# Performance work log

Hardware: AMD Instinct MI355X
Metric: run time of the kernel (lower is better)

## Reference

```python
import jax, jax.numpy as jnp
import numpy as np

DIM = 1024
HEADS = 16
DIM_HEAD = 64
B, N = 4, 2048


def setup_inputs() -> dict:
    key = jax.random.key(0)
    ks = jax.random.split(key, 10)
    s = 0.02
    x = jax.random.normal(ks[0], (B, N, DIM), dtype=jnp.float32)
    Wq = jax.random.normal(ks[1], (DIM, DIM), dtype=jnp.float32) * s
    bq = jnp.zeros((DIM,), dtype=jnp.float32)
    Wk = jax.random.normal(ks[2], (DIM, DIM), dtype=jnp.float32) * s
    bk = jnp.zeros((DIM,), dtype=jnp.float32)
    Wv = jax.random.normal(ks[3], (DIM, DIM), dtype=jnp.float32) * s
    bv = jnp.zeros((DIM,), dtype=jnp.float32)
    Wo = jax.random.normal(ks[4], (DIM, DIM), dtype=jnp.float32) * s
    bo = jnp.zeros((DIM,), dtype=jnp.float32)
    # learnable log-temperature, init = log(dim_head ** -0.5)
    log_temp = jnp.array(np.log(DIM_HEAD ** -0.5), dtype=jnp.float32)
    return {"x": x, "Wq": Wq, "bq": bq, "Wk": Wk, "bk": bk,
            "Wv": Wv, "bv": bv, "Wo": Wo, "bo": bo, "log_temp": log_temp}


def reference(x, Wq, bq, Wk, bk, Wv, bv, Wo, bo, log_temp):
    b, n, _ = x.shape
    # projections (dropout is identity at p=0)
    q = x @ Wq + bq
    k = x @ Wk + bk
    v = x @ Wv + bv
    # [b, n, h*d] -> [b, h, n, d]
    def split_heads(t):
        return t.reshape(b, n, HEADS, DIM_HEAD).transpose(0, 2, 1, 3)
    q, k, v = split_heads(q), split_heads(k), split_heads(v)
    # scaled dot-product scores with learnable temperature
    dots = jnp.einsum('bhid,bhjd->bhij', q, k) * jnp.exp(log_temp)
    # mask out self-attention (diagonal) with -finfo.max
    mask_value = -jnp.finfo(dots.dtype).max
    eye = jnp.eye(n, dtype=bool)
    dots = jnp.where(eye, mask_value, dots)
    attn = jax.nn.softmax(dots, axis=-1)
    out = jnp.einsum('bhij,bhjd->bhid', attn, v)
    # [b, h, n, d] -> [b, n, h*d]
    out = out.transpose(0, 2, 1, 3).reshape(b, n, HEADS * DIM_HEAD)
    return out @ Wo + bo
```

## Files before the change

kernel.cpp:

```cpp
#include <hip/hip_runtime.h>
#include <cmath>

typedef __bf16 bf16_t;
typedef __attribute__((ext_vector_type(8))) __bf16 bf16x8;
typedef __attribute__((ext_vector_type(4))) __bf16 bf16x4;
typedef __attribute__((ext_vector_type(4))) float f32x4;

#define SEQ   2048
#define NHEAD 16
#define DHEAD 64
#define NB    4
#define DIMSZ 1024
#define MROWS 8192

__device__ __forceinline__ void async_copy16(const void* g, void* lds) {
  __builtin_amdgcn_global_load_lds(
      (__attribute__((address_space(1))) void*)(g),
      (__attribute__((address_space(3))) void*)(lds), 16, 0, 0);
}

__device__ __forceinline__ f32x4 f32x4_zero() {
  f32x4 v; v[0] = 0.f; v[1] = 0.f; v[2] = 0.f; v[3] = 0.f; return v;
}

__global__ __launch_bounds__(256) void cvt_x(const float* __restrict__ x,
                                             bf16_t* __restrict__ xb) {
  size_t i = ((size_t)blockIdx.x * 256 + threadIdx.x) * 8;
  float4 f0 = *(const float4*)(x + i);
  float4 f1 = *(const float4*)(x + i + 4);
  bf16x8 o;
  o[0] = (__bf16)f0.x; o[1] = (__bf16)f0.y; o[2] = (__bf16)f0.z; o[3] = (__bf16)f0.w;
  o[4] = (__bf16)f1.x; o[5] = (__bf16)f1.y; o[6] = (__bf16)f1.z; o[7] = (__bf16)f1.w;
  *(bf16x8*)(xb + i) = o;
}

__global__ __launch_bounds__(256) void transpose_w(
    const float* __restrict__ W0, const float* __restrict__ W1,
    const float* __restrict__ W2, const float* __restrict__ W3,
    bf16_t* __restrict__ T0, bf16_t* __restrict__ T1,
    bf16_t* __restrict__ T2, bf16_t* __restrict__ T3) {
  const float* W; bf16_t* T;
  switch (blockIdx.z) {
    case 0: W = W0; T = T0; break;
    case 1: W = W1; T = T1; break;
    case 2: W = W2; T = T2; break;
    default: W = W3; T = T3; break;
  }
  __shared__ float t[32][33];
  int tx = threadIdx.x, ty = threadIdx.y;
  int col = blockIdx.x * 32 + tx;
#pragma unroll
  for (int i = 0; i < 4; i++) {
    int row = blockIdx.y * 32 + ty + i * 8;
    t[ty + i * 8][tx] = W[row * DIMSZ + col];
  }
  __syncthreads();
#pragma unroll
  for (int i = 0; i < 4; i++) {
    int n = blockIdx.x * 32 + ty + i * 8;
    int k = blockIdx.y * 32 + tx;
    T[n * DIMSZ + k] = (bf16_t)t[tx][ty + i * 8];
  }
}

__device__ __forceinline__ void gemm_mainloop(
    const bf16_t* __restrict__ A, const bf16_t* __restrict__ Bt,
    int m0, int n0, f32x4 acc[4][4]) {
  __shared__ __attribute__((aligned(16))) bf16_t As[128 * 64];
  __shared__ __attribute__((aligned(16))) bf16_t Bs[128 * 64];
  const int tid = threadIdx.x;
  const int wid = tid >> 6, lane = tid & 63;
  const int quad = lane >> 4, l16 = lane & 15;
  const int wm = wid & 1, wn = wid >> 1;
  const int srow = lane >> 3;
  const int gchunk = (lane & 7) ^ srow;
#pragma unroll
  for (int r = 0; r < 4; r++)
#pragma unroll
    for (int c = 0; c < 4; c++) acc[r][c] = f32x4_zero();

  for (int k0 = 0; k0 < DIMSZ; k0 += 64) {
#pragma unroll
    for (int c2 = 0; c2 < 4; c2++) {
      int row = c2 * 32 + wid * 8 + srow;
      async_copy16(A + (size_t)(m0 + row) * DIMSZ + k0 + gchunk * 8,
                   &As[(c2 * 32 + wid * 8) * 64]);
      async_copy16(Bt + (size_t)(n0 + row) * DIMSZ + k0 + gchunk * 8,
                   &Bs[(c2 * 32 + wid * 8) * 64]);
    }
    __syncthreads();
#pragma unroll
    for (int kk = 0; kk < 2; kk++) {
      bf16x8 af[4], bf[4];
#pragma unroll
      for (int r = 0; r < 4; r++) {
        int row = wm * 64 + r * 16 + l16;
        int slot = (kk * 4 + quad) ^ (row & 7);
        af[r] = *(const bf16x8*)(As + row * 64 + slot * 8);
      }
#pragma unroll
      for (int c = 0; c < 4; c++) {
        int row = wn * 64 + c * 16 + l16;
        int slot = (kk * 4 + quad) ^ (row & 7);
        bf[c] = *(const bf16x8*)(Bs + row * 64 + slot * 8);
      }
#pragma unroll
      for (int r = 0; r < 4; r++)
#pragma unroll
        for (int c = 0; c < 4; c++)
          acc[r][c] = __builtin_amdgcn_mfma_f32_16x16x32_bf16(af[r], bf[c],
                                                              acc[r][c], 0, 0, 0);
    }
    __syncthreads();
  }
}

__global__ __launch_bounds__(256) void gemm_qkv(
    const bf16_t* __restrict__ A,
    const bf16_t* __restrict__ Wt0, const bf16_t* __restrict__ Wt1,
    const bf16_t* __restrict__ Wt2,
    const float* __restrict__ b0, const float* __restrict__ b1,
    const float* __restrict__ b2,
    bf16_t* __restrict__ o0, bf16_t* __restrict__ o1, bf16_t* __restrict__ o2) {
  const bf16_t* Bt; const float* bias; bf16_t* dst;
  if (blockIdx.z == 0)      { Bt = Wt0; bias = b0; dst = o0; }
  else if (blockIdx.z == 1) { Bt = Wt1; bias = b1; dst = o1; }
  else                      { Bt = Wt2; bias = b2; dst = o2; }
  const int m0 = blockIdx.x * 128, n0 = blockIdx.y * 128;
  f32x4 acc[4][4];
  gemm_mainloop(A, Bt, m0, n0, acc);
  const int lane = threadIdx.x & 63, wid = threadIdx.x >> 6;
  const int quad = lane >> 4, l16 = lane & 15;
  const int wm = wid & 1, wn = wid >> 1;
  if (blockIdx.z == 2) {
#pragma unroll
    for (int c = 0; c < 4; c++) {
      int col = n0 + wn * 64 + c * 16 + l16;
      float bv = bias[col];
      int hh = col >> 6, dd = col & 63;
#pragma unroll
      for (int r = 0; r < 4; r++) {
        int row = m0 + wm * 64 + r * 16 + quad * 4;
        int bb = row >> 11, nn = row & (SEQ - 1);
        bf16x4 pk;
#pragma unroll
        for (int rr = 0; rr < 4; rr++) pk[rr] = (__bf16)(acc[r][c][rr] + bv);
        *(bf16x4*)(dst + ((size_t)(bb * NHEAD + hh) * DHEAD + dd) * SEQ + nn) = pk;
      }
    }
  } else {
#pragma unroll
    for (int c = 0; c < 4; c++) {
      int col = n0 + wn * 64 + c * 16 + l16;
      float bv = bias[col];
      int hh = col >> 6, dd = col & 63;
#pragma unroll
      for (int r = 0; r < 4; r++)
#pragma unroll
        for (int rr = 0; rr < 4; rr++) {
          int row = m0 + wm * 64 + r * 16 + quad * 4 + rr;
          int bb = row >> 11, nn = row & (SEQ - 1);
          dst[(((size_t)(bb * NHEAD + hh) * SEQ + nn) << 6) + dd] =
              (bf16_t)(acc[r][c][rr] + bv);
        }
    }
  }
}

__global__ __launch_bounds__(256) void gemm_out(
    const bf16_t* __restrict__ A, const bf16_t* __restrict__ Bt,
    const float* __restrict__ bias, float* __restrict__ dst) {
  const int m0 = blockIdx.x * 128, n0 = blockIdx.y * 128;
  f32x4 acc[4][4];
  gemm_mainloop(A, Bt, m0, n0, acc);
  const int lane = threadIdx.x & 63, wid = threadIdx.x >> 6;
  const int quad = lane >> 4, l16 = lane & 15;
  const int wm = wid & 1, wn = wid >> 1;
#pragma unroll
  for (int c = 0; c < 4; c++) {
    int col = n0 + wn * 64 + c * 16 + l16;
    float bv = bias[col];
#pragma unroll
    for (int r = 0; r < 4; r++)
#pragma unroll
      for (int rr = 0; rr < 4; rr++) {
        int row = m0 + wm * 64 + r * 16 + quad * 4 + rr;
        dst[(size_t)row * DIMSZ + col] = acc[r][c][rr] + bv;
      }
  }
}

__global__ __launch_bounds__(256, 4) void attn_kernel(
    const bf16_t* __restrict__ qh, const bf16_t* __restrict__ kh,
    const bf16_t* __restrict__ vt, bf16_t* __restrict__ ao,
    const float* __restrict__ log_temp) {
  __shared__ __attribute__((aligned(16))) bf16_t Ks[64 * 64];
  __shared__ __attribute__((aligned(16))) bf16_t Vs[64 * 64];
  __shared__ __attribute__((aligned(16))) bf16_t Ps[4][32 * 64];
  const int tid = threadIdx.x;
  const int wid = tid >> 6, lane = tid & 63;
  const int quad = lane >> 4, l16 = lane & 15;
  const int i0 = blockIdx.x * 128;
  const int h = blockIdx.y, b = blockIdx.z;
  const size_t ho = (size_t)(b * NHEAD + h) * SEQ * DHEAD;
  const bf16_t* Q = qh + ho;
  const float ascale = expf(log_temp[0]) * 1.44269504f;
  const float bshift = 16.0f * 1.44269504f;

  const int irow = i0 + wid * 32;
  bf16x8 qf[2][2];
#pragma unroll
  for (int g = 0; g < 2; g++)
#pragma unroll
    for (int jj = 0; jj < 2; jj++)
      qf[g][jj] = *(const bf16x8*)(Q + (size_t)(irow + g * 16 + l16) * DHEAD +
                                   jj * 32 + quad * 8);

  f32x4 oacc[4][2];
#pragma unroll
  for (int c = 0; c < 4; c++)
#pragma unroll
    for (int g = 0; g < 2; g++) oacc[c][g] = f32x4_zero();
  float lsum[2] = {0.f, 0.f};

  const int srow = lane >> 3;
  const int gch = (lane & 7) ^ srow;
  const bf16_t* kg = kh + ho + (size_t)(wid * 8 + srow) * DHEAD + gch * 8;
  const bf16_t* vg = vt + ho + (size_t)(wid * 8 + srow) * SEQ + gch * 8;
  bf16_t* ksd = &Ks[wid * 8 * 64];
  bf16_t* vsd = &Vs[wid * 8 * 64];
  bf16_t* Pw = Ps[wid];
  const int jdiag = i0 + (wid >> 1) * 64;
  const int x7 = l16 & 7;

  for (int j0 = 0; j0 < SEQ; j0 += 64) {
    async_copy16(kg, ksd);
    async_copy16(kg + 32 * DHEAD, ksd + 32 * 64);
    async_copy16(vg, vsd);
    async_copy16(vg + 32 * SEQ, vsd + 32 * 64);
    kg += 64 * DHEAD;
    vg += 64;
    __syncthreads();

    f32x4 st[4][2];
#pragma unroll
    for (int c = 0; c < 4; c++) {
      const int krow = c * 16 + l16;
      bf16x8 kf0 = *(const bf16x8*)(Ks + krow * 64 + ((0 + quad) ^ x7) * 8);
      bf16x8 kf1 = *(const bf16x8*)(Ks + krow * 64 + ((4 + quad) ^ x7) * 8);
#pragma unroll
      for (int g = 0; g < 2; g++) {
        f32x4 s = f32x4_zero();
        s = __builtin_amdgcn_mfma_f32_16x16x32_bf16(kf0, qf[g][0], s, 0, 0, 0);
        s = __builtin_amdgcn_mfma_f32_16x16x32_bf16(kf1, qf[g][1], s, 0, 0, 0);
        st[c][g] = s;
      }
    }

    const bool isdiag = (j0 == jdiag);
#pragma unroll
    for (int g = 0; g < 2; g++) {
      float ls = 0.f;
      const int ig = irow + g * 16 + l16;
#pragma unroll
      for (int c = 0; c < 4; c++) {
        bf16x4 pk;
#pragma unroll
        for (int rr = 0; rr < 4; rr++) {
          float e = __builtin_amdgcn_exp2f(fmaf(st[c][g][rr], ascale, -bshift));
          if (isdiag && (j0 + c * 16 + quad * 4 + rr == ig)) e = 0.f;
          ls += e;
          pk[rr] = (__bf16)e;
        }
        int slot = (2 * c + (quad >> 1)) ^ x7;
        *(bf16x4*)(Pw + (g * 16 + l16) * 64 + slot * 8 + (quad & 1) * 4) = pk;
      }
      lsum[g] += ls;
    }

    bf16x8 pa[2][2];
#pragma unroll
    for (int g = 0; g < 2; g++) {
      pa[g][0] = *(const bf16x8*)(Pw + (g * 16 + l16) * 64 + ((0 + quad) ^ x7) * 8);
      pa[g][1] = *(const bf16x8*)(Pw + (g * 16 + l16) * 64 + ((4 + quad) ^ x7) * 8);
    }
#pragma unroll
    for (int c = 0; c < 4; c++) {
      const int vrow = c * 16 + l16;
      bf16x8 vb0 = *(const bf16x8*)(Vs + vrow * 64 + ((0 + quad) ^ x7) * 8);
      bf16x8 vb1 = *(const bf16x8*)(Vs + vrow * 64 + ((4 + quad) ^ x7) * 8);
#pragma unroll
      for (int g = 0; g < 2; g++) {
        oacc[c][g] = __builtin_amdgcn_mfma_f32_16x16x32_bf16(pa[g][0], vb0,
                                                             oacc[c][g], 0, 0, 0);
        oacc[c][g] = __builtin_amdgcn_mfma_f32_16x16x32_bf16(pa[g][1], vb1,
                                                             oacc[c][g], 0, 0, 0);
      }
    }
    __syncthreads();
  }

#pragma unroll
  for (int g = 0; g < 2; g++) {
    lsum[g] += __shfl_xor(lsum[g], 16);
    lsum[g] += __shfl_xor(lsum[g], 32);
  }
#pragma unroll
  for (int g = 0; g < 2; g++)
#pragma unroll
    for (int rr = 0; rr < 4; rr++) {
      float lr = __shfl(lsum[g], (lane & 48) | (quad * 4 + rr));
      float inv = 1.f / lr;
      int row = irow + g * 16 + quad * 4 + rr;
#pragma unroll
      for (int c = 0; c < 4; c++) {
        ao[(size_t)(b * SEQ + row) * DIMSZ + h * DHEAD + c * 16 + l16] =
            (bf16_t)(oacc[c][g][rr] * inv);
      }
    }
}

extern "C" void kernel_launch(void* const* d_in, const int* in_sizes, int n_in,
                              void* d_out, int out_size, void* d_ws, size_t ws_size,
                              hipStream_t stream) {
  const float* x  = (const float*)d_in[0];
  const float* Wq = (const float*)d_in[1];
  const float* bq = (const float*)d_in[2];
  const float* Wk = (const float*)d_in[3];
  const float* bk = (const float*)d_in[4];
  const float* Wv = (const float*)d_in[5];
  const float* bv = (const float*)d_in[6];
  const float* Wo = (const float*)d_in[7];
  const float* bo = (const float*)d_in[8];
  const float* lt = (const float*)d_in[9];

  bf16_t* xb  = (bf16_t*)d_ws;
  bf16_t* wtq = xb  + (size_t)MROWS * DIMSZ;
  bf16_t* wtk = wtq + (size_t)DIMSZ * DIMSZ;
  bf16_t* wtv = wtk + (size_t)DIMSZ * DIMSZ;
  bf16_t* wto = wtv + (size_t)DIMSZ * DIMSZ;
  bf16_t* qh  = wto + (size_t)DIMSZ * DIMSZ;
  bf16_t* kh  = qh  + (size_t)MROWS * DIMSZ;
  bf16_t* vh  = kh  + (size_t)MROWS * DIMSZ;
  bf16_t* ao  = xb;

  cvt_x<<<dim3(MROWS * DIMSZ / 2048), dim3(256), 0, stream>>>(x, xb);
  transpose_w<<<dim3(32, 32, 4), dim3(32, 8), 0, stream>>>(
      Wq, Wk, Wv, Wo, wtq, wtk, wtv, wto);
  gemm_qkv<<<dim3(64, 8, 3), dim3(256), 0, stream>>>(
      xb, wtq, wtk, wtv, bq, bk, bv, qh, kh, vh);
  attn_kernel<<<dim3(16, NHEAD, NB), dim3(256), 0, stream>>>(qh, kh, vh, ao, lt);
  gemm_out<<<dim3(64, 8), dim3(256), 0, stream>>>(ao, wto, bo, (float*)d_out);
}
```

Before: 291.7 us.

## Double-buffer LDS tiles in GEMM and attention kernels to overlap loads

Both the GEMM mainloop and the attention KV loop now keep two LDS buffers. The next tile's async global-to-LDS copy is issued right after the barrier, so it overlaps with MFMA work on the current tile, and one barrier per iteration is removed. The attention kernel also precomputes its swizzled LDS offsets, splits the diagonal-mask path into its own branch, and lowers its occupancy hint from 4 to 3; the GEMMs get a min-blocks hint of 2. The cost is double the LDS footprint, which may reduce resident blocks per CU.

New measurement: 279.6 us. -4.2%, faster.

```diff
diff --git a/kernel.cpp b/kernel.cpp
--- a/kernel.cpp
+++ b/kernel.cpp
@@ -66,8 +66,8 @@
 __device__ __forceinline__ void gemm_mainloop(
     const bf16_t* __restrict__ A, const bf16_t* __restrict__ Bt,
     int m0, int n0, f32x4 acc[4][4]) {
-  __shared__ __attribute__((aligned(16))) bf16_t As[128 * 64];
-  __shared__ __attribute__((aligned(16))) bf16_t Bs[128 * 64];
+  __shared__ __attribute__((aligned(16))) bf16_t As[2][128 * 64];
+  __shared__ __attribute__((aligned(16))) bf16_t Bs[2][128 * 64];
   const int tid = threadIdx.x;
   const int wid = tid >> 6, lane = tid & 63;
   const int quad = lane >> 4, l16 = lane & 15;
@@ -79,43 +79,48 @@
 #pragma unroll
     for (int c = 0; c < 4; c++) acc[r][c] = f32x4_zero();
 
-  for (int k0 = 0; k0 < DIMSZ; k0 += 64) {
+  const bf16_t* ag = A + (size_t)(m0 + wid * 8 + srow) * DIMSZ + gchunk * 8;
+  const bf16_t* bg = Bt + (size_t)(n0 + wid * 8 + srow) * DIMSZ + gchunk * 8;
+
+  auto stage = [&](int k0, int buf) {
 #pragma unroll
     for (int c2 = 0; c2 < 4; c2++) {
-      int row = c2 * 32 + wid * 8 + srow;
-      async_copy16(A + (size_t)(m0 + row) * DIMSZ + k0 + gchunk * 8,
-                   &As[(c2 * 32 + wid * 8) * 64]);
-      async_copy16(Bt + (size_t)(n0 + row) * DIMSZ + k0 + gchunk * 8,
-                   &Bs[(c2 * 32 + wid * 8) * 64]);
-    }
+      async_copy16(ag + (size_t)c2 * 32 * DIMSZ + k0, &As[buf][(c2 * 32 + wid * 8) * 64]);
+      async_copy16(bg + (size_t)c2 * 32 * DIMSZ + k0, &Bs[buf][(c2 * 32 + wid * 8) * 64]);
+    }
+  };
+
+  stage(0, 0);
+  for (int it = 0; it < 16; it++) {
+    const int p = it & 1;
     __syncthreads();
+    if (it < 15) stage((it + 1) * 64, 1 - p);
 #pragma unroll
     for (int kk = 0; kk < 2; kk++) {
-      bf16x8 af[4], bf[4];
+      bf16x8 af[4], bfr[4];
 #pragma unroll
       for (int r = 0; r < 4; r++) {
         int row = wm * 64 + r * 16 + l16;
         int slot = (kk * 4 + quad) ^ (row & 7);
-        af[r] = *(const bf16x8*)(As + row * 64 + slot * 8);
+        af[r] = *(const bf16x8*)(&As[p][0] + row * 64 + slot * 8);
       }
 #pragma unroll
       for (int c = 0; c < 4; c++) {
         int row = wn * 64 + c * 16 + l16;
         int slot = (kk * 4 + quad) ^ (row & 7);
-        bf[c] = *(const bf16x8*)(Bs + row * 64 + slot * 8);
+        bfr[c] = *(const bf16x8*)(&Bs[p][0] + row * 64 + slot * 8);
       }
 #pragma unroll
       for (int r = 0; r < 4; r++)
 #pragma unroll
         for (int c = 0; c < 4; c++)
-          acc[r][c] = __builtin_amdgcn_mfma_f32_16x16x32_bf16(af[r], bf[c],
+          acc[r][c] = __builtin_amdgcn_mfma_f32_16x16x32_bf16(af[r], bfr[c],
                                                               acc[r][c], 0, 0, 0);
     }
-    __syncthreads();
-  }
-}
-
-__global__ __launch_bounds__(256) void gemm_qkv(
+  }
+}
+
+__global__ __launch_bounds__(256, 2) void gemm_qkv(
     const bf16_t* __restrict__ A,
     const bf16_t* __restrict__ Wt0, const bf16_t* __restrict__ Wt1,
     const bf16_t* __restrict__ Wt2,
@@ -167,7 +172,7 @@
   }
 }
 
-__global__ __launch_bounds__(256) void gemm_out(
+__global__ __launch_bounds__(256, 2) void gemm_out(
     const bf16_t* __restrict__ A, const bf16_t* __restrict__ Bt,
     const float* __restrict__ bias, float* __restrict__ dst) {
   const int m0 = blockIdx.x * 128, n0 = blockIdx.y * 128;
@@ -190,12 +195,12 @@
   }
 }
 
-__global__ __launch_bounds__(256, 4) void attn_kernel(
+__global__ __launch_bounds__(256, 3) void attn_kernel(
     const bf16_t* __restrict__ qh, const bf16_t* __restrict__ kh,
     const bf16_t* __restrict__ vt, bf16_t* __restrict__ ao,
     const float* __restrict__ log_temp) {
-  __shared__ __attribute__((aligned(16))) bf16_t Ks[64 * 64];
-  __shared__ __attribute__((aligned(16))) bf16_t Vs[64 * 64];
+  __shared__ __attribute__((aligned(16))) bf16_t Ks[2][64 * 64];
+  __shared__ __attribute__((aligned(16))) bf16_t Vs[2][64 * 64];
   __shared__ __attribute__((aligned(16))) bf16_t Ps[4][32 * 64];
   const int tid = threadIdx.x;
   const int wid = tid >> 6, lane = tid & 63;
@@ -227,27 +232,57 @@
   const int gch = (lane & 7) ^ srow;
   const bf16_t* kg = kh + ho + (size_t)(wid * 8 + srow) * DHEAD + gch * 8;
   const bf16_t* vg = vt + ho + (size_t)(wid * 8 + srow) * SEQ + gch * 8;
-  bf16_t* ksd = &Ks[wid * 8 * 64];
-  bf16_t* vsd = &Vs[wid * 8 * 64];
   bf16_t* Pw = Ps[wid];
-  const int jdiag = i0 + (wid >> 1) * 64;
   const int x7 = l16 & 7;
-
-  for (int j0 = 0; j0 < SEQ; j0 += 64) {
-    async_copy16(kg, ksd);
-    async_copy16(kg + 32 * DHEAD, ksd + 32 * 64);
-    async_copy16(vg, vsd);
-    async_copy16(vg + 32 * SEQ, vsd + 32 * 64);
-    kg += 64 * DHEAD;
-    vg += 64;
+  const int jdiag_t = blockIdx.x * 2 + (wid >> 1);
+
+  int kvoff[4][2];
+#pragma unroll
+  for (int c = 0; c < 4; c++)
+#pragma unroll
+    for (int kk = 0; kk < 2; kk++) {
+      int row = c * 16 + l16;
+      kvoff[c][kk] = row * 64 + (((kk * 4) + quad) ^ x7) * 8;
+    }
+  bf16_t* pwa[2][4];
+#pragma unroll
+  for (int g = 0; g < 2; g++)
+#pragma unroll
+    for (int c = 0; c < 4; c++) {
+      int slot = (2 * c + (quad >> 1)) ^ x7;
+      pwa[g][c] = Pw + (g * 16 + l16) * 64 + slot * 8 + (quad & 1) * 4;
+    }
+  const bf16_t* paa[2][2];
+#pragma unroll
+  for (int g = 0; g < 2; g++)
+#pragma unroll
+    for (int kk = 0; kk < 2; kk++)
+      paa[g][kk] = Pw + (g * 16 + l16) * 64 + (((kk * 4) + quad) ^ x7) * 8;
+
+  auto stage = [&](int jt, int buf) {
+    const bf16_t* kp = kg + (size_t)jt * 64 * DHEAD;
+    const bf16_t* vp = vg + jt * 64;
+    bf16_t* kd = &Ks[buf][wid * 8 * 64];
+    bf16_t* vd = &Vs[buf][wid * 8 * 64];
+    async_copy16(kp, kd);
+    async_copy16(kp + 32 * DHEAD, kd + 32 * 64);
+    async_copy16(vp, vd);
+    async_copy16(vp + 32 * SEQ, vd + 32 * 64);
+  };
+
+  stage(0, 0);
+  for (int jt = 0; jt < SEQ / 64; jt++) {
+    const int p = jt & 1;
     __syncthreads();
+    if (jt + 1 < SEQ / 64) stage(jt + 1, 1 - p);
+    const bf16_t* Kp = &Ks[p][0];
+    const bf16_t* Vp = &Vs[p][0];
 
     f32x4 st[4][2];
 #pragma unroll
     for (int c = 0; c < 4; c++) {
-      const int krow = c * 16 + l16;
-      bf16x8 kf0 = *(const bf16x8*)(Ks + krow * 64 + ((0 + quad) ^ x7) * 8);
-      bf16x8 kf1 = *(const bf16x8*)(Ks + krow * 64 + ((4 + quad) ^ x7) * 8);
+      bf16x8 kf0 = *(const bf16x8*)(Kp + kvoff[c][0]);
+      bf16x8 kf1 = *(const bf16x8*)(Kp + kvoff[c][1]);
 #pragma unroll
       for (int g = 0; g < 2; g++) {
         f32x4 s = f32x4_zero();
@@ -257,38 +292,55 @@
       }
     }
 
-    const bool isdiag = (j0 == jdiag);
+    const int j0 = jt * 64;
+    if (jt == jdiag_t) {
+#pragma unroll
+      for (int g = 0; g < 2; g++) {
+        float ls = 0.f;
+        const int ig = irow + g * 16 + l16;
+#pragma unroll
+        for (int c = 0; c < 4; c++) {
+          bf16x4 pk;
+#pragma unroll
+          for (int rr = 0; rr < 4; rr++) {
+            float e = __builtin_amdgcn_exp2f(fmaf(st[c][g][rr], ascale, -bshift));
+            if (j0 + c * 16 + quad * 4 + rr == ig) e = 0.f;
+            ls += e;
+            pk[rr] = (__bf16)e;
+          }
+          *(bf16x4*)pwa[g][c] = pk;
+        }
+        lsum[g] += ls;
+      }
+    } else {
+#pragma unroll
+      for (int g = 0; g < 2; g++) {
+        float ls = 0.f;
+#pragma unroll
+        for (int c = 0; c < 4; c++) {
+          bf16x4 pk;
+#pragma unroll
+          for (int rr = 0; rr < 4; rr++) {
+            float e = __builtin_amdgcn_exp2f(fmaf(st[c][g][rr], ascale, -bshift));
+            ls += e;
+            pk[rr] = (__bf16)e;
+          }
+          *(bf16x4*)pwa[g][c] = pk;
+        }
+        lsum[g] += ls;
+      }
+    }
+
+    bf16x8 pa[2][2];
 #pragma unroll
     for (int g = 0; g < 2; g++) {
-      float ls = 0.f;
-      const int ig = irow + g * 16 + l16;
-#pragma unroll
-      for (int c = 0; c < 4; c++) {
-        bf16x4 pk;
-#pragma unroll
-        for (int rr = 0; rr < 4; rr++) {
-          float e = __builtin_amdgcn_exp2f(fmaf(st[c][g][rr], ascale, -bshift));
-          if (isdiag && (j0 + c * 16 + quad * 4 + rr == ig)) e = 0.f;
-          ls += e;
-          pk[rr] = (__bf16)e;
-        }
-        int slot = (2 * c + (quad >> 1)) ^ x7;
-        *(bf16x4*)(Pw + (g * 16 + l16) * 64 + slot * 8 + (quad & 1) * 4) = pk;
-      }
-      lsum[g] += ls;
-    }
-
-    bf16x8 pa[2][2];
-#pragma unroll
-    for (int g = 0; g < 2; g++) {
-      pa[g][0] = *(const bf16x8*)(Pw + (g * 16 + l16) * 64 + ((0 + quad) ^ x7) * 8);
-      pa[g][1] = *(const bf16x8*)(Pw + (g * 16 + l16) * 64 + ((4 + quad) ^ x7) * 8);
+      pa[g][0] = *(const bf16x8*)paa[g][0];
+      pa[g][1] = *(const bf16x8*)paa[g][1];
     }
 #pragma unroll
     for (int c = 0; c < 4; c++) {
-      const int vrow = c * 16 + l16;
-      bf16x8 vb0 = *(const bf16x8*)(Vs + vrow * 64 + ((0 + quad) ^ x7) * 8);
-      bf16x8 vb1 = *(const bf16x8*)(Vs + vrow * 64 + ((4 + quad) ^ x7) * 8);
+      bf16x8 vb0 = *(const bf16x8*)(Vp + kvoff[c][0]);
+      bf16x8 vb1 = *(const bf16x8*)(Vp + kvoff[c][1]);
 #pragma unroll
       for (int g = 0; g < 2; g++) {
         oacc[c][g] = __builtin_amdgcn_mfma_f32_16x16x32_bf16(pa[g][0], vb0,
@@ -297,7 +349,6 @@
                                                              oacc[c][g], 0, 0, 0);
       }
     }
-    __syncthreads();
   }
 
 #pragma unroll
```
